# Performance work log

Measured on AMD Instinct MI355X. Metric: run time of the kernel, lower is better.

The kernel has to match this reference:

```python
import jax, jax.numpy as jnp
import numpy as np

N, NCB, DIM, CB_SIZE = 16384, 8, 32, 1024


def setup_inputs() -> dict:
    key = jax.random.key(0)
    k1, k2, k3 = jax.random.split(key, 3)
    x = jax.random.normal(k1, (N, NCB, DIM), dtype=jnp.float32)
    codebook = jax.random.normal(k2, (NCB, CB_SIZE, DIM), dtype=jnp.float32)
    rate_bias = jax.random.normal(k3, (NCB, CB_SIZE), dtype=jnp.float32)
    return {"x": x, "codebook": codebook, "rate_bias": rate_bias}


def reference(x, codebook, rate_bias):
    # x: (N, ncb, dim), codebook: (ncb, cb_size, dim)
    x_sq = jnp.sum(x * x, axis=-1, keepdims=True)            # (N, ncb, 1)
    cb_sq = jnp.sum(codebook * codebook, axis=-1)            # (ncb, cb_size)
    cross = jnp.einsum('nkd,kcd->nkc', x, codebook)          # (N, ncb, cb_size)
    dist = x_sq + cb_sq - 2.0 * cross                        # (N, ncb, cb_size)
    dist = dist + rate_bias                                  # rate_bias broadcast
    index = jnp.argmin(dist, axis=-1, keepdims=True)         # (N, ncb, 1)
    one_hot = jax.nn.one_hot(index[..., 0], CB_SIZE, dtype=dist.dtype)  # (N, ncb, cb_size)
    x_hat = jnp.einsum('nkc,kcd->nkd', one_hot, codebook)    # (N, ncb, dim)
    return (x_hat, one_hot, index)
```

## Files before the change

### kernel.cpp

```cpp
#include <hip/hip_runtime.h>

#define NN 16384
#define NCB 8
#define DIM 32
#define CB 1024
#define RPB 512
#define QC 256
#define TILE 64
#define NT (QC / TILE)

__global__ __launch_bounds__(256) void vq_csq(const float* __restrict__ cb,
                                              const float* __restrict__ rb,
                                              float* __restrict__ out) {
    int i = blockIdx.x * 256 + threadIdx.x;
    if (i >= NCB * CB) return;
    const float4* c4 = reinterpret_cast<const float4*>(cb + (size_t)i * DIM);
    float s0 = 0.f, s1 = 0.f, s2 = 0.f, s3 = 0.f;
#pragma unroll
    for (int j = 0; j < 8; ++j) {
        float4 v = c4[j];
        s0 = fmaf(v.x, v.x, s0);
        s1 = fmaf(v.y, v.y, s1);
        s2 = fmaf(v.z, v.z, s2);
        s3 = fmaf(v.w, v.w, s3);
    }
    out[i] = ((s0 + s1) + (s2 + s3)) + rb[i];
}

__global__ __launch_bounds__(512, 2) void vq_fused(
    const float* __restrict__ x, const float* __restrict__ cb,
    const float* __restrict__ csqb, float* __restrict__ xhat,
    float* __restrict__ onehot, float* __restrict__ idxf) {
    __shared__ float4 tiles[8][2][TILE * 8];
    __shared__ float pd[4][RPB];
    __shared__ int pi[4][RPB];

    const int tid = threadIdx.x;
    const int w = tid >> 6;
    const int lane = tid & 63;
    const int rh = w >> 2;
    const int q = w & 3;
    const int k = blockIdx.x & (NCB - 1);
    const int n0 = (blockIdx.x >> 3) * RPB;

    const float4* cbk4 =
        reinterpret_cast<const float4*>(cb + (size_t)k * CB * DIM);
    const float* cqk = csqb + (size_t)k * CB;

    const int rbase = rh * 256 + lane * 4;
    float4 xr[4][8];
    float xsq[4];
#pragma unroll
    for (int j = 0; j < 4; ++j) {
        const int n = n0 + rbase + j;
        const float4* xp =
            reinterpret_cast<const float4*>(x + ((size_t)n * NCB + k) * DIM);
#pragma unroll
        for (int jj = 0; jj < 8; ++jj) xr[j][jj] = xp[jj];
        float q0 = 0.f, q1 = 0.f, q2 = 0.f, q3 = 0.f;
#pragma unroll
        for (int jj = 0; jj < 8; ++jj) {
            q0 = fmaf(xr[j][jj].x, xr[j][jj].x, q0);
            q1 = fmaf(xr[j][jj].y, xr[j][jj].y, q1);
            q2 = fmaf(xr[j][jj].z, xr[j][jj].z, q2);
            q3 = fmaf(xr[j][jj].w, xr[j][jj].w, q3);
        }
        xsq[j] = (q0 + q1) + (q2 + q3);
    }

    float best[4];
    int bi[4];
#pragma unroll
    for (int j = 0; j < 4; ++j) {
        best[j] = 3.4028235e38f;
        bi[j] = 0;
    }

    const int qbase = q * QC;
    float4 st[8];
    float cq_cur, cq_nxt = 0.f;
#pragma unroll
    for (int i = 0; i < 8; ++i) st[i] = cbk4[(size_t)qbase * 8 + i * 64 + lane];
    cq_cur = cqk[qbase + lane];
#pragma unroll
    for (int i = 0; i < 8; ++i) tiles[w][0][i * 64 + lane] = st[i];

    float4* oh4 = reinterpret_cast<float4*>(onehot);
    const float4 z4 = make_float4(0.f, 0.f, 0.f, 0.f);

    for (int t = 0; t < NT; ++t) {
        const int b = t & 1;
        if (t < NT - 1) {
#pragma unroll
            for (int i = 0; i < 8; ++i)
                st[i] = cbk4[((size_t)qbase + (t + 1) * TILE) * 8 + i * 64 +
                             lane];
            cq_nxt = cqk[qbase + (t + 1) * TILE + lane];
        }

        const float4* buf = &tiles[w][b][0];
#pragma unroll 2
        for (int c = 0; c < TILE; ++c) {
            {
                const int zrow = n0 + w * 64 + t * 16 + (c >> 2);
                float4* rp = oh4 + ((size_t)zrow * NCB + k) * 256;
                rp[(c & 3) * 64 + lane] = z4;
            }

            const float cqv = __int_as_float(
                __builtin_amdgcn_readlane(__float_as_int(cq_cur), c));
            float4 A[8];
#pragma unroll
            for (int jj = 0; jj < 8; ++jj) A[jj] = buf[c * 8 + jj];
            const int cg = qbase + t * TILE + c;

#pragma unroll
            for (int j = 0; j < 4; ++j) {
                float d0 = 0.f, d1 = 0.f, d2 = 0.f, d3 = 0.f;
#pragma unroll
                for (int jj = 0; jj < 8; ++jj) {
                    d0 = fmaf(xr[j][jj].x, A[jj].x, d0);
                    d1 = fmaf(xr[j][jj].y, A[jj].y, d1);
                    d2 = fmaf(xr[j][jj].z, A[jj].z, d2);
                    d3 = fmaf(xr[j][jj].w, A[jj].w, d3);
                }
                const float dot = (d0 + d1) + (d2 + d3);
                const float dist = fmaf(-2.f, dot, xsq[j] + cqv);
                if (dist < best[j]) {
                    best[j] = dist;
                    bi[j] = cg;
                }
            }
        }

        if (t < NT - 1) {
#pragma unroll
            for (int i = 0; i < 8; ++i) tiles[w][b ^ 1][i * 64 + lane] = st[i];
            cq_cur = cq_nxt;
        }
    }

#pragma unroll
    for (int j = 0; j < 4; ++j) {
        pd[q][rbase + j] = best[j];
        pi[q][rbase + j] = bi[j];
    }
    __syncthreads();

    {
        const int r = tid;
        float bd = pd[0][r];
        int bx = pi[0][r];
#pragma unroll
        for (int qq = 1; qq < 4; ++qq) {
            const float dq = pd[qq][r];
            const int iq = pi[qq][r];
            if (dq < bd) {
                bd = dq;
                bx = iq;
            }
        }
        const int n = n0 + r;
        idxf[(size_t)n * NCB + k] = (float)bx;
        const float4* src = cbk4 + (size_t)bx * 8;
        float4* dst =
            reinterpret_cast<float4*>(xhat + ((size_t)n * NCB + k) * DIM);
#pragma unroll
        for (int jj = 0; jj < 8; ++jj) dst[jj] = src[jj];
        onehot[((size_t)n * NCB + k) * CB + bx] = 1.0f;
    }
}

extern "C" void kernel_launch(void* const* d_in, const int* in_sizes, int n_in,
                              void* d_out, int out_size, void* d_ws,
                              size_t ws_size, hipStream_t stream) {
    const float* x = (const float*)d_in[0];
    const float* cb = (const float*)d_in[1];
    const float* rb = (const float*)d_in[2];

    float* out = (float*)d_out;
    float* xhat = out;
    float* onehot = out + (size_t)NN * NCB * DIM;
    float* idxf = onehot + (size_t)NN * NCB * CB;

    float* csqb = (float*)d_ws;

    vq_csq<<<(NCB * CB + 255) / 256, 256, 0, stream>>>(cb, rb, csqb);
    vq_fused<<<(NN / RPB) * NCB, 512, 0, stream>>>(x, cb, csqb, xhat, onehot,
                                                   idxf);
}
```

Before: 178.2 us.

## Zero one-hot in contiguous per-block chunks and scatter ones after a grid sync

Each block now zero-fills a contiguous 2 MB slice of the one-hot output, chosen by block id, instead of the strided rows that belong to its own (row, codebook) pairs. Because those slices no longer line up with each block's results, the argmin indices go to a workspace buffer. After a cooperative grid-wide sync, each thread writes its 1.0 into the one-hot array. The goal is more sequential, better-coalesced write streams for the dominant 512 MB zero fill. In exchange it requires a cooperative launch with all 256 blocks co-resident, adds a grid barrier, and adds a second pass of scattered stores.

```diff
diff --git a/kernel.cpp b/kernel.cpp
--- a/kernel.cpp
+++ b/kernel.cpp
@@ -1,4 +1,7 @@
 #include <hip/hip_runtime.h>
+#include <hip/hip_cooperative_groups.h>
+
+namespace cg = cooperative_groups;
 
 #define NN 16384
 #define NCB 8
@@ -7,7 +10,7 @@
 #define RPB 512
 #define QC 256
 #define TILE 64
-#define NT (QC / TILE)
+#define NTL (QC / TILE)
 
 __global__ __launch_bounds__(256) void vq_csq(const float* __restrict__ cb,
                                               const float* __restrict__ rb,
@@ -30,7 +33,8 @@
 __global__ __launch_bounds__(512, 2) void vq_fused(
     const float* __restrict__ x, const float* __restrict__ cb,
     const float* __restrict__ csqb, float* __restrict__ xhat,
-    float* __restrict__ onehot, float* __restrict__ idxf) {
+    float* __restrict__ onehot, float* __restrict__ idxf,
+    int* __restrict__ bi_ws) {
     __shared__ float4 tiles[8][2][TILE * 8];
     __shared__ float pd[4][RPB];
     __shared__ int pi[4][RPB];
@@ -40,8 +44,9 @@
     const int lane = tid & 63;
     const int rh = w >> 2;
     const int q = w & 3;
-    const int k = blockIdx.x & (NCB - 1);
-    const int n0 = (blockIdx.x >> 3) * RPB;
+    const int bid = blockIdx.x;
+    const int k = bid & (NCB - 1);
+    const int n0 = (bid >> 3) * RPB;
 
     const float4* cbk4 =
         reinterpret_cast<const float4*>(cb + (size_t)k * CB * DIM);
@@ -85,12 +90,13 @@
 #pragma unroll
     for (int i = 0; i < 8; ++i) tiles[w][0][i * 64 + lane] = st[i];
 
-    float4* oh4 = reinterpret_cast<float4*>(onehot);
+    float4* zbase = reinterpret_cast<float4*>(onehot) + (size_t)bid * 131072 +
+                    (size_t)w * 16384;
     const float4 z4 = make_float4(0.f, 0.f, 0.f, 0.f);
 
-    for (int t = 0; t < NT; ++t) {
+    for (int t = 0; t < NTL; ++t) {
         const int b = t & 1;
-        if (t < NT - 1) {
+        if (t < NTL - 1) {
 #pragma unroll
             for (int i = 0; i < 8; ++i)
                 st[i] = cbk4[((size_t)qbase + (t + 1) * TILE) * 8 + i * 64 +
@@ -101,11 +107,7 @@
         const float4* buf = &tiles[w][b][0];
 #pragma unroll 2
         for (int c = 0; c < TILE; ++c) {
-            {
-                const int zrow = n0 + w * 64 + t * 16 + (c >> 2);
-                float4* rp = oh4 + ((size_t)zrow * NCB + k) * 256;
-                rp[(c & 3) * 64 + lane] = z4;
-            }
+            zbase[(size_t)(t * TILE + c) * 64 + lane] = z4;
 
             const float cqv = __int_as_float(
                 __builtin_amdgcn_readlane(__float_as_int(cq_cur), c));
@@ -133,7 +135,7 @@
             }
         }
 
-        if (t < NT - 1) {
+        if (t < NTL - 1) {
 #pragma unroll
             for (int i = 0; i < 8; ++i) tiles[w][b ^ 1][i * 64 + lane] = st[i];
             cq_cur = cq_nxt;
@@ -167,7 +169,17 @@
             reinterpret_cast<float4*>(xhat + ((size_t)n * NCB + k) * DIM);
 #pragma unroll
         for (int jj = 0; jj < 8; ++jj) dst[jj] = src[jj];
-        onehot[((size_t)n * NCB + k) * CB + bx] = 1.0f;
+        __hip_atomic_store(&bi_ws[(size_t)n * NCB + k], bx, __ATOMIC_RELAXED,
+                           __HIP_MEMORY_SCOPE_AGENT);
+    }
+
+    cg::this_grid().sync();
+
+    {
+        const int p = bid * 512 + tid;
+        const int bv = __hip_atomic_load(&bi_ws[p], __ATOMIC_RELAXED,
+                                         __HIP_MEMORY_SCOPE_AGENT);
+        onehot[(size_t)p * CB + bv] = 1.0f;
     }
 }
 
@@ -184,8 +196,13 @@
     float* idxf = onehot + (size_t)NN * NCB * CB;
 
     float* csqb = (float*)d_ws;
+    int* bi_ws = (int*)((char*)d_ws + 65536);
 
     vq_csq<<<(NCB * CB + 255) / 256, 256, 0, stream>>>(cb, rb, csqb);
-    vq_fused<<<(NN / RPB) * NCB, 512, 0, stream>>>(x, cb, csqb, xhat, onehot,
-                                                   idxf);
+
+    void* args[] = {(void*)&x,      (void*)&cb,   (void*)&csqb,
+                    (void*)&xhat,   (void*)&onehot, (void*)&idxf,
+                    (void*)&bi_ws};
+    hipLaunchCooperativeKernel((void*)vq_fused, dim3((NN / RPB) * NCB),
+                               dim3(512), args, 0, stream);
 }
```

New measurement: 219.6 us. +23.2%, slower.

## Use direct global-to-LDS loads, packed FP32 FMA, and batched one-hot zeroing

Applied to the files above, without the earlier changes.

Codebook tiles now go straight into LDS with global_load_lds instead of through registers, with manual vmcnt waits and a smaller tile of 32 entries. The dot products use v_pk_fma_f32 on split x halves to double FMA throughput per instruction. The one-hot zero stores are grouped into a batch before each tile instead of being interleaved with compute, and occupancy is lowered to one block per SIMD group. The hand-counted vmcnt values and the missing waits between waves writing and reading LDS are fragile and could cause races or stalls.

```diff
diff --git a/kernel.cpp b/kernel.cpp
--- a/kernel.cpp
+++ b/kernel.cpp
@@ -1,4 +1,7 @@
 #include <hip/hip_runtime.h>
+
+typedef float f32x2 __attribute__((ext_vector_type(2)));
+typedef float f32x4 __attribute__((ext_vector_type(4)));
 
 #define NN 16384
 #define NCB 8
@@ -6,8 +9,20 @@
 #define CB 1024
 #define RPB 512
 #define QC 256
-#define TILE 64
-#define NT (QC / TILE)
+#define TILE 32
+#define NTL (QC / TILE)
+
+__device__ __forceinline__ void gload_lds16(const void* g, void* l) {
+    __builtin_amdgcn_global_load_lds(
+        (const __attribute__((address_space(1))) unsigned int*)g,
+        (__attribute__((address_space(3))) unsigned int*)l, 16, 0, 0);
+}
+
+__device__ __forceinline__ f32x2 pkfma(f32x2 a, f32x2 b, f32x2 c) {
+    f32x2 d = c;
+    asm("v_pk_fma_f32 %0, %1, %2, %0" : "+v"(d) : "v"(a), "v"(b));
+    return d;
+}
 
 __global__ __launch_bounds__(256) void vq_csq(const float* __restrict__ cb,
                                               const float* __restrict__ rb,
@@ -27,11 +42,11 @@
     out[i] = ((s0 + s1) + (s2 + s3)) + rb[i];
 }
 
-__global__ __launch_bounds__(512, 2) void vq_fused(
+__global__ __launch_bounds__(512, 1) void vq_fused(
     const float* __restrict__ x, const float* __restrict__ cb,
     const float* __restrict__ csqb, float* __restrict__ xhat,
     float* __restrict__ onehot, float* __restrict__ idxf) {
-    __shared__ float4 tiles[8][2][TILE * 8];
+    __shared__ f32x4 tiles[8][2][TILE * 8];
     __shared__ float pd[4][RPB];
     __shared__ int pi[4][RPB];
 
@@ -43,29 +58,35 @@
     const int k = blockIdx.x & (NCB - 1);
     const int n0 = (blockIdx.x >> 3) * RPB;
 
-    const float4* cbk4 =
-        reinterpret_cast<const float4*>(cb + (size_t)k * CB * DIM);
+    const f32x4* cbk4 =
+        reinterpret_cast<const f32x4*>(cb + (size_t)k * CB * DIM);
     const float* cqk = csqb + (size_t)k * CB;
 
     const int rbase = rh * 256 + lane * 4;
-    float4 xr[4][8];
+    f32x2 xlo[4][8], xhi[4][8];
     float xsq[4];
 #pragma unroll
     for (int j = 0; j < 4; ++j) {
         const int n = n0 + rbase + j;
-        const float4* xp =
-            reinterpret_cast<const float4*>(x + ((size_t)n * NCB + k) * DIM);
-#pragma unroll
-        for (int jj = 0; jj < 8; ++jj) xr[j][jj] = xp[jj];
+        const f32x4* xp =
+            reinterpret_cast<const f32x4*>(x + ((size_t)n * NCB + k) * DIM);
+        f32x4 xt[8];
+#pragma unroll
+        for (int jj = 0; jj < 8; ++jj) xt[jj] = xp[jj];
         float q0 = 0.f, q1 = 0.f, q2 = 0.f, q3 = 0.f;
 #pragma unroll
         for (int jj = 0; jj < 8; ++jj) {
-            q0 = fmaf(xr[j][jj].x, xr[j][jj].x, q0);
-            q1 = fmaf(xr[j][jj].y, xr[j][jj].y, q1);
-            q2 = fmaf(xr[j][jj].z, xr[j][jj].z, q2);
-            q3 = fmaf(xr[j][jj].w, xr[j][jj].w, q3);
+            q0 = fmaf(xt[jj].x, xt[jj].x, q0);
+            q1 = fmaf(xt[jj].y, xt[jj].y, q1);
+            q2 = fmaf(xt[jj].z, xt[jj].z, q2);
+            q3 = fmaf(xt[jj].w, xt[jj].w, q3);
         }
         xsq[j] = (q0 + q1) + (q2 + q3);
+#pragma unroll
+        for (int jj = 0; jj < 8; ++jj) {
+            xlo[j][jj] = __builtin_shufflevector(xt[jj], xt[jj], 0, 1);
+            xhi[j][jj] = __builtin_shufflevector(xt[jj], xt[jj], 2, 3);
+        }
     }
 
     float best[4];
@@ -77,66 +98,83 @@
     }
 
     const int qbase = q * QC;
-    float4 st[8];
-    float cq_cur, cq_nxt = 0.f;
-#pragma unroll
-    for (int i = 0; i < 8; ++i) st[i] = cbk4[(size_t)qbase * 8 + i * 64 + lane];
-    cq_cur = cqk[qbase + lane];
-#pragma unroll
-    for (int i = 0; i < 8; ++i) tiles[w][0][i * 64 + lane] = st[i];
+    float cqall[4];
+#pragma unroll
+    for (int i = 0; i < 4; ++i) cqall[i] = cqk[qbase + i * 64 + lane];
+
+    __builtin_amdgcn_sched_barrier(0);
+#pragma unroll
+    for (int i = 0; i < 4; ++i)
+        gload_lds16(cbk4 + (size_t)qbase * 8 + i * 64 + lane,
+                    &tiles[w][0][i * 64]);
+    __builtin_amdgcn_sched_barrier(0);
 
     float4* oh4 = reinterpret_cast<float4*>(onehot);
     const float4 z4 = make_float4(0.f, 0.f, 0.f, 0.f);
 
-    for (int t = 0; t < NT; ++t) {
-        const int b = t & 1;
-        if (t < NT - 1) {
-#pragma unroll
-            for (int i = 0; i < 8; ++i)
-                st[i] = cbk4[((size_t)qbase + (t + 1) * TILE) * 8 + i * 64 +
-                             lane];
-            cq_nxt = cqk[qbase + (t + 1) * TILE + lane];
-        }
-
-        const float4* buf = &tiles[w][b][0];
+#pragma unroll
+    for (int th = 0; th < 4; ++th) {
+        const float cql = cqall[th];
+        for (int sub = 0; sub < 2; ++sub) {
+            const int t = th * 2 + sub;
+            const int b = t & 1;
+
+            {
+                const int zb = n0 + w * 64 + t * 8;
+#pragma unroll
+                for (int rr = 0; rr < 8; ++rr) {
+                    float4* rp = oh4 + ((size_t)(zb + rr) * NCB + k) * 256;
+#pragma unroll
+                    for (int s = 0; s < 4; ++s) rp[s * 64 + lane] = z4;
+                }
+            }
+            __builtin_amdgcn_sched_barrier(0);
+
+            if (t < NTL - 1) {
+#pragma unroll
+                for (int i = 0; i < 4; ++i)
+                    gload_lds16(
+                        cbk4 + ((size_t)qbase + (t + 1) * TILE) * 8 + i * 64 +
+                            lane,
+                        &tiles[w][b ^ 1][i * 64]);
+                __builtin_amdgcn_sched_barrier(0);
+                asm volatile("s_waitcnt vmcnt(36)" ::: "memory");
+            } else {
+                asm volatile("s_waitcnt vmcnt(32)" ::: "memory");
+            }
+            __builtin_amdgcn_sched_barrier(0);
+
+            const f32x4* buf = &tiles[w][b][0];
 #pragma unroll 2
-        for (int c = 0; c < TILE; ++c) {
-            {
-                const int zrow = n0 + w * 64 + t * 16 + (c >> 2);
-                float4* rp = oh4 + ((size_t)zrow * NCB + k) * 256;
-                rp[(c & 3) * 64 + lane] = z4;
-            }
-
-            const float cqv = __int_as_float(
-                __builtin_amdgcn_readlane(__float_as_int(cq_cur), c));
-            float4 A[8];
-#pragma unroll
-            for (int jj = 0; jj < 8; ++jj) A[jj] = buf[c * 8 + jj];
-            const int cg = qbase + t * TILE + c;
-
-#pragma unroll
-            for (int j = 0; j < 4; ++j) {
-                float d0 = 0.f, d1 = 0.f, d2 = 0.f, d3 = 0.f;
-#pragma unroll
-                for (int jj = 0; jj < 8; ++jj) {
-                    d0 = fmaf(xr[j][jj].x, A[jj].x, d0);
-                    d1 = fmaf(xr[j][jj].y, A[jj].y, d1);
-                    d2 = fmaf(xr[j][jj].z, A[jj].z, d2);
-                    d3 = fmaf(xr[j][jj].w, A[jj].w, d3);
+            for (int c = 0; c < TILE; ++c) {
+                const float cqv = __int_as_float(__builtin_amdgcn_readlane(
+                    __float_as_int(cql), (sub << 5) + c));
+                f32x4 A[8];
+#pragma unroll
+                for (int jj = 0; jj < 8; ++jj) A[jj] = buf[c * 8 + jj];
+                const int cg = qbase + t * TILE + c;
+
+#pragma unroll
+                for (int j = 0; j < 4; ++j) {
+                    f32x2 acc01 = {0.f, 0.f}, acc23 = {0.f, 0.f};
+#pragma unroll
+                    for (int jj = 0; jj < 8; ++jj) {
+                        const f32x2 alo =
+                            __builtin_shufflevector(A[jj], A[jj], 0, 1);
+                        const f32x2 ahi =
+                            __builtin_shufflevector(A[jj], A[jj], 2, 3);
+                        acc01 = pkfma(xlo[j][jj], alo, acc01);
+                        acc23 = pkfma(xhi[j][jj], ahi, acc23);
+                    }
+                    const float dot =
+                        (acc01.x + acc01.y) + (acc23.x + acc23.y);
+                    const float dist = fmaf(-2.f, dot, xsq[j] + cqv);
+                    if (dist < best[j]) {
+                        best[j] = dist;
+                        bi[j] = cg;
+                    }
                 }
-                const float dot = (d0 + d1) + (d2 + d3);
-                const float dist = fmaf(-2.f, dot, xsq[j] + cqv);
-                if (dist < best[j]) {
-                    best[j] = dist;
-                    bi[j] = cg;
-                }
-            }
-        }
-
-        if (t < NT - 1) {
-#pragma unroll
-            for (int i = 0; i < 8; ++i) tiles[w][b ^ 1][i * 64 + lane] = st[i];
-            cq_cur = cq_nxt;
+            }
         }
     }
 
@@ -162,9 +200,9 @@
         }
         const int n = n0 + r;
         idxf[(size_t)n * NCB + k] = (float)bx;
-        const float4* src = cbk4 + (size_t)bx * 8;
-        float4* dst =
-            reinterpret_cast<float4*>(xhat + ((size_t)n * NCB + k) * DIM);
+        const f32x4* src = cbk4 + (size_t)bx * 8;
+        f32x4* dst =
+            reinterpret_cast<f32x4*>(xhat + ((size_t)n * NCB + k) * DIM);
 #pragma unroll
         for (int jj = 0; jj < 8; ++jj) dst[jj] = src[jj];
         onehot[((size_t)n * NCB + k) * CB + bx] = 1.0f;
```

Result: no change. 175.4 us (-1.6%).

## Drop LDS codebook tiling, use wave-uniform scalar loads, halve rows per block

Applied to the files above, without the earlier changes.

Removes the double-buffered LDS codebook tiles. Each wave now reads codebook entries straight from global memory at a wave-uniform address, with the quarter index made uniform via readfirstlane so the compiler can emit scalar loads. Rows per block drop from 512 to 256, so each thread handles 2 rows instead of 4 and the grid doubles. The one-hot zero fill is reindexed to match. This saves LDS traffic and barriers and may raise occupancy, at the cost of less register reuse of each codebook entry and more codebook reloads overall.

```diff
diff --git a/kernel.cpp b/kernel.cpp
--- a/kernel.cpp
+++ b/kernel.cpp
@@ -1,24 +1,24 @@
 #include <hip/hip_runtime.h>
+
+typedef float f32x4 __attribute__((ext_vector_type(4)));
 
 #define NN 16384
 #define NCB 8
 #define DIM 32
 #define CB 1024
-#define RPB 512
+#define RPB 256
 #define QC 256
-#define TILE 64
-#define NT (QC / TILE)
 
 __global__ __launch_bounds__(256) void vq_csq(const float* __restrict__ cb,
                                               const float* __restrict__ rb,
                                               float* __restrict__ out) {
     int i = blockIdx.x * 256 + threadIdx.x;
     if (i >= NCB * CB) return;
-    const float4* c4 = reinterpret_cast<const float4*>(cb + (size_t)i * DIM);
+    const f32x4* c4 = (const f32x4*)(cb + (size_t)i * DIM);
     float s0 = 0.f, s1 = 0.f, s2 = 0.f, s3 = 0.f;
 #pragma unroll
     for (int j = 0; j < 8; ++j) {
-        float4 v = c4[j];
+        f32x4 v = c4[j];
         s0 = fmaf(v.x, v.x, s0);
         s1 = fmaf(v.y, v.y, s1);
         s2 = fmaf(v.z, v.z, s2);
@@ -31,7 +31,6 @@
     const float* __restrict__ x, const float* __restrict__ cb,
     const float* __restrict__ csqb, float* __restrict__ xhat,
     float* __restrict__ onehot, float* __restrict__ idxf) {
-    __shared__ float4 tiles[8][2][TILE * 8];
     __shared__ float pd[4][RPB];
     __shared__ int pi[4][RPB];
 
@@ -39,22 +38,21 @@
     const int w = tid >> 6;
     const int lane = tid & 63;
     const int rh = w >> 2;
-    const int q = w & 3;
+    const int q = __builtin_amdgcn_readfirstlane(w & 3);
     const int k = blockIdx.x & (NCB - 1);
     const int n0 = (blockIdx.x >> 3) * RPB;
 
-    const float4* cbk4 =
-        reinterpret_cast<const float4*>(cb + (size_t)k * CB * DIM);
+    const float* cbk = cb + (size_t)k * CB * DIM;
+    const f32x4* cbk4 = (const f32x4*)cbk;
     const float* cqk = csqb + (size_t)k * CB;
 
-    const int rbase = rh * 256 + lane * 4;
-    float4 xr[4][8];
-    float xsq[4];
+    const int rbase = rh * 128 + lane * 2;
+    f32x4 xr[2][8];
+    float xsq[2];
 #pragma unroll
-    for (int j = 0; j < 4; ++j) {
+    for (int j = 0; j < 2; ++j) {
         const int n = n0 + rbase + j;
-        const float4* xp =
-            reinterpret_cast<const float4*>(x + ((size_t)n * NCB + k) * DIM);
+        const f32x4* xp = (const f32x4*)(x + ((size_t)n * NCB + k) * DIM);
 #pragma unroll
         for (int jj = 0; jj < 8; ++jj) xr[j][jj] = xp[jj];
         float q0 = 0.f, q1 = 0.f, q2 = 0.f, q3 = 0.f;
@@ -68,54 +66,47 @@
         xsq[j] = (q0 + q1) + (q2 + q3);
     }
 
-    float best[4];
-    int bi[4];
+    float best[2];
+    int bi[2];
 #pragma unroll
-    for (int j = 0; j < 4; ++j) {
+    for (int j = 0; j < 2; ++j) {
         best[j] = 3.4028235e38f;
         bi[j] = 0;
     }
 
     const int qbase = q * QC;
-    float4 st[8];
-    float cq_cur, cq_nxt = 0.f;
+    const float* cbe = cbk + (size_t)qbase * DIM;
+    float cqall[4];
 #pragma unroll
-    for (int i = 0; i < 8; ++i) st[i] = cbk4[(size_t)qbase * 8 + i * 64 + lane];
-    cq_cur = cqk[qbase + lane];
+    for (int i = 0; i < 4; ++i) cqall[i] = cqk[qbase + i * 64 + lane];
+
+    float4* oh4 = (float4*)onehot;
+    const float4 z4 = {0.f, 0.f, 0.f, 0.f};
+
 #pragma unroll
-    for (int i = 0; i < 8; ++i) tiles[w][0][i * 64 + lane] = st[i];
+    for (int g = 0; g < 4; ++g) {
+        const float cql = cqall[g];
+#pragma unroll 2
+        for (int cc = 0; cc < 64; ++cc) {
+            const int e = g * 64 + cc;
 
-    float4* oh4 = reinterpret_cast<float4*>(onehot);
-    const float4 z4 = make_float4(0.f, 0.f, 0.f, 0.f);
-
-    for (int t = 0; t < NT; ++t) {
-        const int b = t & 1;
-        if (t < NT - 1) {
-#pragma unroll
-            for (int i = 0; i < 8; ++i)
-                st[i] = cbk4[((size_t)qbase + (t + 1) * TILE) * 8 + i * 64 +
-                             lane];
-            cq_nxt = cqk[qbase + (t + 1) * TILE + lane];
-        }
-
-        const float4* buf = &tiles[w][b][0];
-#pragma unroll 2
-        for (int c = 0; c < TILE; ++c) {
-            {
-                const int zrow = n0 + w * 64 + t * 16 + (c >> 2);
-                float4* rp = oh4 + ((size_t)zrow * NCB + k) * 256;
-                rp[(c & 3) * 64 + lane] = z4;
+            if ((e & 1) == 0) {
+                const int s = e >> 1;
+                oh4[((size_t)(n0 + w * 32 + (s >> 2)) * NCB + k) * 256 +
+                    (s & 3) * 64 + lane] = z4;
             }
 
+            const f32x4* ep = (const f32x4*)(cbe + (size_t)e * DIM);
+            f32x4 A[8];
+#pragma unroll
+            for (int jj = 0; jj < 8; ++jj) A[jj] = ep[jj];
+
             const float cqv = __int_as_float(
-                __builtin_amdgcn_readlane(__float_as_int(cq_cur), c));
-            float4 A[8];
-#pragma unroll
-            for (int jj = 0; jj < 8; ++jj) A[jj] = buf[c * 8 + jj];
-            const int cg = qbase + t * TILE + c;
+                __builtin_amdgcn_readlane(__float_as_int(cql), cc));
+            const int cg = qbase + e;
 
 #pragma unroll
-            for (int j = 0; j < 4; ++j) {
+            for (int j = 0; j < 2; ++j) {
                 float d0 = 0.f, d1 = 0.f, d2 = 0.f, d3 = 0.f;
 #pragma unroll
                 for (int jj = 0; jj < 8; ++jj) {
@@ -132,22 +123,16 @@
                 }
             }
         }
-
-        if (t < NT - 1) {
-#pragma unroll
-            for (int i = 0; i < 8; ++i) tiles[w][b ^ 1][i * 64 + lane] = st[i];
-            cq_cur = cq_nxt;
-        }
     }
 
 #pragma unroll
-    for (int j = 0; j < 4; ++j) {
+    for (int j = 0; j < 2; ++j) {
         pd[q][rbase + j] = best[j];
         pi[q][rbase + j] = bi[j];
     }
     __syncthreads();
 
-    {
+    if (tid < RPB) {
         const int r = tid;
         float bd = pd[0][r];
         int bx = pi[0][r];
@@ -162,9 +147,8 @@
         }
         const int n = n0 + r;
         idxf[(size_t)n * NCB + k] = (float)bx;
-        const float4* src = cbk4 + (size_t)bx * 8;
-        float4* dst =
-            reinterpret_cast<float4*>(xhat + ((size_t)n * NCB + k) * DIM);
+        const f32x4* src = cbk4 + (size_t)bx * 8;
+        f32x4* dst = (f32x4*)(xhat + ((size_t)n * NCB + k) * DIM);
 #pragma unroll
         for (int jj = 0; jj < 8; ++jj) dst[jj] = src[jj];
         onehot[((size_t)n * NCB + k) * CB + bx] = 1.0f;
```

New measurement: 207.1 us. +16.2%, slower.
